# Kernel tuning notes

Measured on AMD Instinct MI355X. Metric: run time of the kernel, lower is better.

## Reference

```python
import jax, jax.numpy as jnp
import numpy as np

EPS = 1e-5
B, C_IN, T_IN = 512, 12, 5000
NF, HID, LAT = 32, 64, 32


def setup_inputs() -> dict:
    key = jax.random.key(0)
    ks = jax.random.split(key, 12)
    inp = {
        "x": jax.random.normal(ks[0], (B, C_IN, T_IN), dtype=jnp.float32),
        # conv stack
        "conv1_w": jax.random.normal(ks[1], (32, C_IN, 50), dtype=jnp.float32) * 0.05,
        "conv1_b": jnp.zeros((32,), dtype=jnp.float32),
        "bn1_g": jnp.ones((32,), dtype=jnp.float32),
        "bn1_b": jnp.zeros((32,), dtype=jnp.float32),
        "conv2_w": jax.random.normal(ks[2], (NF, 32, 25), dtype=jnp.float32) * 0.05,
        "conv2_b": jnp.zeros((NF,), dtype=jnp.float32),
        "bn2_g": jnp.ones((NF,), dtype=jnp.float32),
        "bn2_b": jnp.zeros((NF,), dtype=jnp.float32),
        # input projection + layernorm
        "proj_w": jax.random.normal(ks[3], (LAT, NF), dtype=jnp.float32) * 0.1,
        "proj_b": jnp.zeros((LAT,), dtype=jnp.float32),
        "ln_g": jnp.ones((LAT,), dtype=jnp.float32),
        "ln_b": jnp.zeros((LAT,), dtype=jnp.float32),
        # PLRNN recurrence params
        "A": jnp.eye(LAT, dtype=jnp.float32) * 0.9,
        "W": jax.random.normal(ks[4], (LAT, HID), dtype=jnp.float32) * 0.1,
        "h_bias": jnp.zeros((HID,), dtype=jnp.float32),
        # output projection
        "out_w": jax.random.normal(ks[5], (LAT, LAT), dtype=jnp.float32) * 0.1,
        "out_b": jnp.zeros((LAT,), dtype=jnp.float32),
    }
    return inp


def _conv1d(x, w, b, stride):
    # x: [B, C, T], w: [O, I, K]
    y = jax.lax.conv_general_dilated(
        x, w, window_strides=(stride,), padding="VALID",
        dimension_numbers=("NCH", "OIH", "NCH"))
    return y + b[None, :, None]


def _batchnorm_train(x, g, b):
    # training-mode BN over (batch, time) per channel; x: [B, C, T]
    mean = jnp.mean(x, axis=(0, 2), keepdims=True)
    var = jnp.mean((x - mean) ** 2, axis=(0, 2), keepdims=True)
    return (x - mean) * jax.lax.rsqrt(var + EPS) * g[None, :, None] + b[None, :, None]


def _layernorm(x, g, b):
    mean = jnp.mean(x, axis=-1, keepdims=True)
    var = jnp.mean((x - mean) ** 2, axis=-1, keepdims=True)
    return (x - mean) * jax.lax.rsqrt(var + EPS) * g + b


def reference(x, conv1_w, conv1_b, bn1_g, bn1_b, conv2_w, conv2_b, bn2_g, bn2_b,
              proj_w, proj_b, ln_g, ln_b, A, W, h_bias, out_w, out_b):
    # conv front-end
    y = jax.nn.relu(_batchnorm_train(_conv1d(x, conv1_w, conv1_b, 10), bn1_g, bn1_b))
    y = jax.nn.relu(_batchnorm_train(_conv1d(y, conv2_w, conv2_b, 5), bn2_g, bn2_b))
    y = jnp.transpose(y, (0, 2, 1))  # [B, T, NF], T = 95

    # input projection + LN, vectorized over all timesteps
    xt = _layernorm(jnp.einsum("btf,lf->btl", y, proj_w) + proj_b, ln_g, ln_b)  # [B, T, L]
    xs = jnp.transpose(xt, (1, 0, 2))  # [T, B, L] for scan

    def step(h, x_t):
        # h: [B, L]
        linear = h @ A.T
        nonlinear = jax.nn.relu(h @ W + h_bias) @ W.T
        h_new = linear + nonlinear + x_t
        return h_new, h_new

    h0 = jnp.zeros((x.shape[0], A.shape[0]), dtype=x.dtype)
    _, outputs = jax.lax.scan(step, h0, xs)  # [T, B, L]

    pooled = jnp.mean(outputs, axis=0)  # [B, L]
    return pooled @ out_w.T + out_b
```

## Files before the change

kernel.cpp:

```cpp
#include <hip/hip_runtime.h>

#define NB    512
#define CIN   12
#define TIN   5000
#define C1    32
#define T1    496
#define T2    95
#define LATD  32
#define HIDD  64

#define OFS_STATS 0
#define OFS_W1P   256
#define OFS_W2P   19456
#define OFS_Y1    45056
#define OFS_Y2    8171520
#define OFS_XS    OFS_Y1

__global__ void prep_kernel(const float* __restrict__ w1, const float* __restrict__ w2,
                            float* __restrict__ ws) {
    int idx = blockIdx.x * 256 + threadIdx.x;
    if (idx < 256) ws[idx] = 0.f;
    int j = idx - 256;
    if (j >= 0 && j < 19200) {
        int ic = j / 1600, r = j % 1600;
        int p = r / 160, rr = r % 160, jj = rr / 32, oc = rr % 32;
        ws[OFS_W1P + j] = w1[oc * 600 + ic * 50 + 10 * jj + p];
    }
    int j2 = idx - 19456;
    if (j2 >= 0 && j2 < 25600) {
        int ic = j2 / 800, r = j2 % 800;
        int p = r / 160, rr = r % 160, jj = rr / 32, oc = rr % 32;
        ws[OFS_W2P + j2] = w2[oc * 800 + ic * 25 + 5 * jj + p];
    }
}

__global__ __launch_bounds__(256, 4) void conv1_kernel(const float* __restrict__ x,
                                                       const float* __restrict__ b1,
                                                       float* __restrict__ ws) {
    const float* w1p = ws + OFS_W1P;
    float* y1 = ws + OFS_Y1;
    float* stats = ws + OFS_STATS;
    int b  = blockIdx.x >> 1;
    int t0 = (blockIdx.x & 1) * 256;
    int tid = threadIdx.x;
    int ocg = tid & 7, tg = tid >> 3;
    int oc0 = ocg * 4, lt0 = tg * 8;

    __shared__ __align__(16) float xs_s[2][2680];
    __shared__ __align__(16) float ws_s[2][1600];
    __shared__ float sred[256];

    float acc[4][8];
#pragma unroll
    for (int a = 0; a < 4; ++a)
#pragma unroll
        for (int c = 0; c < 8; ++c) acc[a][c] = 0.f;

    const float* xb = x + (size_t)b * (CIN * TIN) + t0 * 10;
    int nvalid = TIN - t0 * 10;

    float4 px[3];
    float4 pw[2];

    auto fetch = [&](int ic) {
#pragma unroll
        for (int j = 0; j < 3; ++j) {
            int i = tid + j * 256;
            if (i < 650) {
                int src = 4 * i;
                const float* gp = xb + ic * TIN + src;
                float4 v;
                if (src + 4 <= nvalid) {
                    v = *(const float4*)gp;
                } else {
                    v.x = (src + 0 < nvalid) ? gp[0] : 0.f;
                    v.y = (src + 1 < nvalid) ? gp[1] : 0.f;
                    v.z = (src + 2 < nvalid) ? gp[2] : 0.f;
                    v.w = (src + 3 < nvalid) ? gp[3] : 0.f;
                }
                px[j] = v;
            }
        }
#pragma unroll
        for (int j = 0; j < 2; ++j) {
            int i = tid + j * 256;
            if (i < 400) pw[j] = *(const float4*)(w1p + ic * 1600 + 4 * i);
        }
    };

    fetch(0);
    for (int ic = 0; ic < CIN; ++ic) {
        int cur = ic & 1;
        __syncthreads();
#pragma unroll
        for (int j = 0; j < 3; ++j) {
            int i = tid + j * 256;
            if (i < 650) {
                int g = 4 * i;
                int col = g / 10, p = g - 10 * col;
                float vals[4] = {px[j].x, px[j].y, px[j].z, px[j].w};
#pragma unroll
                for (int m = 0; m < 4; ++m) {
                    int pm = p + m;
                    int rr = (pm >= 10) ? pm - 10 : pm;
                    int cc = col + ((pm >= 10) ? 1 : 0);
                    xs_s[cur][rr * 268 + cc] = vals[m];
                }
            }
        }
#pragma unroll
        for (int j = 0; j < 2; ++j) {
            int i = tid + j * 256;
            if (i < 400) *(float4*)&ws_s[cur][4 * i] = pw[j];
        }
        if (ic + 1 < CIN) fetch(ic + 1);
        __syncthreads();

#pragma unroll 2
        for (int p = 0; p < 10; ++p) {
            const float* xr = &xs_s[cur][p * 268 + 8 * tg];
            float4 xa = *(const float4*)(xr);
            float4 xbv = *(const float4*)(xr + 4);
            float4 xc = *(const float4*)(xr + 8);
            float xv[12] = {xa.x, xa.y, xa.z, xa.w,
                            xbv.x, xbv.y, xbv.z, xbv.w,
                            xc.x, xc.y, xc.z, xc.w};
            const float* wr = &ws_s[cur][p * 160 + oc0];
            float4 w0 = *(const float4*)(wr);
            float4 w1v = *(const float4*)(wr + 32);
            float4 w2v = *(const float4*)(wr + 64);
            float4 w3v = *(const float4*)(wr + 96);
            float4 w4v = *(const float4*)(wr + 128);
            float wj[5][4] = {{w0.x, w0.y, w0.z, w0.w},
                              {w1v.x, w1v.y, w1v.z, w1v.w},
                              {w2v.x, w2v.y, w2v.z, w2v.w},
                              {w3v.x, w3v.y, w3v.z, w3v.w},
                              {w4v.x, w4v.y, w4v.z, w4v.w}};
#pragma unroll
            for (int j = 0; j < 5; ++j)
#pragma unroll
                for (int jt = 0; jt < 8; ++jt) {
                    float xx = xv[jt + j];
#pragma unroll
                    for (int jo = 0; jo < 4; ++jo)
                        acc[jo][jt] = fmaf(wj[j][jo], xx, acc[jo][jt]);
                }
        }
    }

    float bias[4];
#pragma unroll
    for (int jo = 0; jo < 4; ++jo) bias[jo] = b1[oc0 + jo];

    bool tvalid = (t0 + lt0) <= (T1 - 8);
    float psum[4], psq[4];
#pragma unroll
    for (int jo = 0; jo < 4; ++jo) {
        float s = 0.f, q = 0.f;
        if (tvalid) {
            float tmp[8];
#pragma unroll
            for (int jt = 0; jt < 8; ++jt) {
                float v = acc[jo][jt] + bias[jo];
                tmp[jt] = v; s += v; q = fmaf(v, v, q);
            }
            float* yrow = y1 + (size_t)(b * 32 + oc0 + jo) * T1 + t0 + lt0;
            float4 o0; o0.x = tmp[0]; o0.y = tmp[1]; o0.z = tmp[2]; o0.w = tmp[3];
            float4 o1; o1.x = tmp[4]; o1.y = tmp[5]; o1.z = tmp[6]; o1.w = tmp[7];
            *(float4*)yrow       = o0;
            *(float4*)(yrow + 4) = o1;
        }
        psum[jo] = s; psq[jo] = q;
    }
#pragma unroll
    for (int off = 32; off >= 8; off >>= 1) {
#pragma unroll
        for (int jo = 0; jo < 4; ++jo) {
            psum[jo] += __shfl_down(psum[jo], off, 64);
            psq[jo]  += __shfl_down(psq[jo],  off, 64);
        }
    }
    int lane = tid & 63, wvi = tid >> 6;
    if (lane < 8) {
#pragma unroll
        for (int jo = 0; jo < 4; ++jo) {
            sred[((wvi * 8 + lane) * 4 + jo) * 2 + 0] = psum[jo];
            sred[((wvi * 8 + lane) * 4 + jo) * 2 + 1] = psq[jo];
        }
    }
    __syncthreads();
    if (tid < 64) {
        int oc = tid >> 1, which = tid & 1;
        int og = oc >> 2, jo = oc & 3;
        float v = 0.f;
#pragma unroll
        for (int w = 0; w < 4; ++w)
            v += sred[((w * 8 + og) * 4 + jo) * 2 + which];
        atomicAdd(&stats[which * 32 + oc], v);
    }
}

__global__ __launch_bounds__(192, 2) void conv2_kernel(const float* __restrict__ b2,
                                                       const float* __restrict__ g1,
                                                       const float* __restrict__ be1,
                                                       float* __restrict__ ws) {
    const float* w2p = ws + OFS_W2P;
    const float* y1 = ws + OFS_Y1;
    float* y2 = ws + OFS_Y2;
    float* stats = ws + OFS_STATS;
    int b = blockIdx.x;
    int tid = threadIdx.x;
    int ocg = tid & 7, tg = tid >> 3;
    int oc0 = ocg * 4, lt0 = tg * 4;

    __shared__ __align__(16) float a1s[2][500];
    __shared__ __align__(16) float w2s[2][800];
    __shared__ float sred[192];
    __shared__ float bns[64];

    if (tid < 32) {
        float mean = stats[tid] * (1.f / 253952.f);
        float var  = stats[32 + tid] * (1.f / 253952.f) - mean * mean;
        float s = g1[tid] * rsqrtf(var + 1e-5f);
        bns[tid]      = s;
        bns[32 + tid] = be1[tid] - mean * s;
    }

    float acc[4][4];
#pragma unroll
    for (int a = 0; a < 4; ++a)
#pragma unroll
        for (int c = 0; c < 4; ++c) acc[a][c] = 0.f;

    float4 py, pw0, pw1;
    auto fetch = [&](int ic) {
        const float* yrow = y1 + (size_t)(b * 32 + ic) * T1;
        if (tid < 124) py = *(const float4*)(yrow + 4 * tid);
        pw0 = *(const float4*)(w2p + ic * 800 + 4 * tid);
        if (tid < 8) pw1 = *(const float4*)(w2p + ic * 800 + 4 * (tid + 192));
    };

    fetch(0);
    for (int ic = 0; ic < 32; ++ic) {
        int cur = ic & 1;
        __syncthreads();
        if (tid < 124) {
            float s1 = bns[ic], sh1 = bns[32 + ic];
            float4 v = py;
            float vals[4];
            vals[0] = fmaxf(fmaf(v.x, s1, sh1), 0.f);
            vals[1] = fmaxf(fmaf(v.y, s1, sh1), 0.f);
            vals[2] = fmaxf(fmaf(v.z, s1, sh1), 0.f);
            vals[3] = fmaxf(fmaf(v.w, s1, sh1), 0.f);
            int g = 4 * tid;
            int col = g / 5, p = g - 5 * col;
#pragma unroll
            for (int m = 0; m < 4; ++m) {
                int pm = p + m;
                int rr = (pm >= 5) ? pm - 5 : pm;
                int cc = col + ((pm >= 5) ? 1 : 0);
                a1s[cur][rr * 100 + cc] = vals[m];
            }
        }
        *(float4*)&w2s[cur][4 * tid] = pw0;
        if (tid < 8) *(float4*)&w2s[cur][4 * (tid + 192)] = pw1;
        if (ic + 1 < 32) fetch(ic + 1);
        __syncthreads();

#pragma unroll 2
        for (int p = 0; p < 5; ++p) {
            const float* xr = &a1s[cur][p * 100 + 4 * tg];
            float4 xa = *(const float4*)(xr);
            float4 xbv = *(const float4*)(xr + 4);
            float xv[8] = {xa.x, xa.y, xa.z, xa.w, xbv.x, xbv.y, xbv.z, xbv.w};
            const float* wr = &w2s[cur][p * 160 + oc0];
            float4 w0 = *(const float4*)(wr);
            float4 w1v = *(const float4*)(wr + 32);
            float4 w2v = *(const float4*)(wr + 64);
            float4 w3v = *(const float4*)(wr + 96);
            float4 w4v = *(const float4*)(wr + 128);
            float wj[5][4] = {{w0.x, w0.y, w0.z, w0.w},
                              {w1v.x, w1v.y, w1v.z, w1v.w},
                              {w2v.x, w2v.y, w2v.z, w2v.w},
                              {w3v.x, w3v.y, w3v.z, w3v.w},
                              {w4v.x, w4v.y, w4v.z, w4v.w}};
#pragma unroll
            for (int j = 0; j < 5; ++j)
#pragma unroll
                for (int jt = 0; jt < 4; ++jt) {
                    float xx = xv[jt + j];
#pragma unroll
                    for (int jo = 0; jo < 4; ++jo)
                        acc[jo][jt] = fmaf(wj[j][jo], xx, acc[jo][jt]);
                }
        }
    }

    float bias[4];
#pragma unroll
    for (int jo = 0; jo < 4; ++jo) bias[jo] = b2[oc0 + jo];

    float psum[4], psq[4];
#pragma unroll
    for (int jo = 0; jo < 4; ++jo) {
        float s = 0.f, q = 0.f;
#pragma unroll
        for (int jt = 0; jt < 4; ++jt) {
            int t2 = lt0 + jt;
            if (t2 < T2) {
                float v = acc[jo][jt] + bias[jo];
                y2[(size_t)(b * 32 + oc0 + jo) * T2 + t2] = v;
                s += v; q = fmaf(v, v, q);
            }
        }
        psum[jo] = s; psq[jo] = q;
    }
#pragma unroll
    for (int off = 32; off >= 8; off >>= 1) {
#pragma unroll
        for (int jo = 0; jo < 4; ++jo) {
            psum[jo] += __shfl_down(psum[jo], off, 64);
            psq[jo]  += __shfl_down(psq[jo],  off, 64);
        }
    }
    int lane = tid & 63, wvi = tid >> 6;
    if (lane < 8) {
#pragma unroll
        for (int jo = 0; jo < 4; ++jo) {
            sred[((wvi * 8 + lane) * 4 + jo) * 2 + 0] = psum[jo];
            sred[((wvi * 8 + lane) * 4 + jo) * 2 + 1] = psq[jo];
        }
    }
    __syncthreads();
    if (tid < 64) {
        int oc = tid >> 1, which = tid & 1;
        int og = oc >> 2, jo = oc & 3;
        float v = 0.f;
#pragma unroll
        for (int w = 0; w < 3; ++w)
            v += sred[((w * 8 + og) * 4 + jo) * 2 + which];
        atomicAdd(&stats[64 + which * 32 + oc], v);
    }
}

__global__ __launch_bounds__(256, 2) void proj_kernel(const float* __restrict__ g2,
                                                      const float* __restrict__ be2,
                                                      const float* __restrict__ pw,
                                                      const float* __restrict__ pb,
                                                      const float* __restrict__ lng,
                                                      const float* __restrict__ lnb,
                                                      float* __restrict__ ws) {
    int b = blockIdx.x;
    int tid = threadIdx.x;
    __shared__ float a2s[3040];
    __shared__ float pws[1056];
    __shared__ float bns2[64];
    const float* stats = ws + OFS_STATS;
    const float* y2 = ws + OFS_Y2 + (size_t)b * (32 * T2);
    float* xsg = ws + OFS_XS;

    if (tid < 32) {
        float mean = stats[64 + tid] * (1.f / 48640.f);
        float var  = stats[96 + tid] * (1.f / 48640.f) - mean * mean;
        float s = g2[tid] * rsqrtf(var + 1e-5f);
        bns2[tid]      = s;
        bns2[32 + tid] = be2[tid] - mean * s;
    }
    __syncthreads();

    for (int f = 0; f < 32; ++f) {
        float s2  = bns2[f];
        float sh2 = bns2[32 + f];
        if (tid < T2)
            a2s[f * T2 + tid] = fmaxf(fmaf(y2[f * T2 + tid], s2, sh2), 0.f);
    }
    for (int i = tid; i < 1024; i += 256)
        pws[(i >> 5) * 33 + (i & 31)] = pw[i];

    int l = tid & 31, ts = tid >> 5;
    float pbv = pb[l], lg = lng[l], lb = lnb[l];
    __syncthreads();

    for (int it = 0; it < 12; ++it) {
        int t = ts + 8 * it;
        if (t < T2) {
            float v = pbv;
#pragma unroll
            for (int f = 0; f < 32; ++f)
                v = fmaf(a2s[f * T2 + t], pws[l * 33 + f], v);
            float sum = v;
#pragma unroll
            for (int off = 16; off >= 1; off >>= 1) sum += __shfl_xor(sum, off, 64);
            float mean = sum * (1.f / 32.f);
            float d = v - mean;
            float q = d * d;
#pragma unroll
            for (int off = 16; off >= 1; off >>= 1) q += __shfl_xor(q, off, 64);
            float o = d * rsqrtf(q * (1.f / 32.f) + 1e-5f) * lg + lb;
            xsg[(size_t)t * (NB * 32) + b * 32 + l] = o;
        }
    }
}

__global__ __launch_bounds__(64)
__attribute__((amdgpu_waves_per_eu(1, 1)))
void scan_kernel(const float* __restrict__ Am,
                 const float* __restrict__ Wm,
                 const float* __restrict__ hbp,
                 const float* __restrict__ ow,
                 const float* __restrict__ ob,
                 const float* __restrict__ ws,
                 float* __restrict__ out) {
    int b = blockIdx.x;
    int lane = threadIdx.x;
    int l = lane & 31, half = lane >> 5;
    __shared__ __align__(16) float hs[32];
    __shared__ __align__(16) float hds[64];
    __shared__ float ows[1056];

    float Wc[32], WT[32], Ah[16];
#pragma unroll
    for (int j = 0; j < 32; ++j) Wc[j] = Wm[j * HIDD + lane];
#pragma unroll
    for (int m = 0; m < 32; ++m) WT[m] = Wm[l * HIDD + half * 32 + m];
#pragma unroll
    for (int j = 0; j < 16; ++j) Ah[j] = Am[l * 32 + half * 16 + j];
    float hbv = hbp[lane];
    for (int i = lane; i < 1024; i += 64)
        ows[(i >> 5) * 33 + (i & 31)] = ow[i];

    const float* xsg = ws + OFS_XS + b * 32;
    if (lane < 32) hs[l] = 0.f;
    float xv = xsg[l];
    float pool = 0.f;
    __syncthreads();

    for (int t = 0; t < T2; ++t) {
        __syncthreads();
        float4 hv[8];
#pragma unroll
        for (int q = 0; q < 8; ++q) hv[q] = *(const float4*)&hs[4 * q];
        float a0 = hbv, a1 = 0.f, a2 = 0.f, a3 = 0.f;
#pragma unroll
        for (int q = 0; q < 8; ++q) {
            a0 = fmaf(Wc[4 * q + 0], hv[q].x, a0);
            a1 = fmaf(Wc[4 * q + 1], hv[q].y, a1);
            a2 = fmaf(Wc[4 * q + 2], hv[q].z, a2);
            a3 = fmaf(Wc[4 * q + 3], hv[q].w, a3);
        }
        float hid = fmaxf((a0 + a1) + (a2 + a3), 0.f);
        float4 hl[4];
#pragma unroll
        for (int q = 0; q < 4; ++q) hl[q] = *(const float4*)&hs[half * 16 + 4 * q];
        float l0 = 0.f, l1 = 0.f;
#pragma unroll
        for (int q = 0; q < 4; ++q) {
            l0 = fmaf(Ah[4 * q + 0], hl[q].x, l0);
            l1 = fmaf(Ah[4 * q + 1], hl[q].y, l1);
            l0 = fmaf(Ah[4 * q + 2], hl[q].z, l0);
            l1 = fmaf(Ah[4 * q + 3], hl[q].w, l1);
        }
        float lin = l0 + l1;
        hds[lane] = hid;
        __syncthreads();
        float n0 = 0.f, n1 = 0.f, n2 = 0.f, n3 = 0.f;
#pragma unroll
        for (int q = 0; q < 8; ++q) {
            float4 d4 = *(const float4*)&hds[half * 32 + 4 * q];
            n0 = fmaf(WT[4 * q + 0], d4.x, n0);
            n1 = fmaf(WT[4 * q + 1], d4.y, n1);
            n2 = fmaf(WT[4 * q + 2], d4.z, n2);
            n3 = fmaf(WT[4 * q + 3], d4.w, n3);
        }
        float part = (n0 + n1) + (n2 + n3) + lin;
        part += __shfl_xor(part, 32, 64);
        float hnew = part + xv;
        pool += hnew;
        if (t + 1 < T2) xv = xsg[(size_t)(t + 1) * (NB * 32) + l];
        if (lane < 32) hs[l] = hnew;
    }

    __syncthreads();
    if (lane < 32) hs[l] = pool * (1.f / 95.f);
    __syncthreads();
    if (lane < 32) {
        float4 p0 = *(const float4*)&hs[0];
        float4 p1 = *(const float4*)&hs[4];
        float4 p2 = *(const float4*)&hs[8];
        float4 p3 = *(const float4*)&hs[12];
        float4 p4 = *(const float4*)&hs[16];
        float4 p5 = *(const float4*)&hs[20];
        float4 p6 = *(const float4*)&hs[24];
        float4 p7 = *(const float4*)&hs[28];
        float o = ob[l];
        const float* owr = &ows[l * 33];
        o = fmaf(owr[0],  p0.x, o); o = fmaf(owr[1],  p0.y, o);
        o = fmaf(owr[2],  p0.z, o); o = fmaf(owr[3],  p0.w, o);
        o = fmaf(owr[4],  p1.x, o); o = fmaf(owr[5],  p1.y, o);
        o = fmaf(owr[6],  p1.z, o); o = fmaf(owr[7],  p1.w, o);
        o = fmaf(owr[8],  p2.x, o); o = fmaf(owr[9],  p2.y, o);
        o = fmaf(owr[10], p2.z, o); o = fmaf(owr[11], p2.w, o);
        o = fmaf(owr[12], p3.x, o); o = fmaf(owr[13], p3.y, o);
        o = fmaf(owr[14], p3.z, o); o = fmaf(owr[15], p3.w, o);
        o = fmaf(owr[16], p4.x, o); o = fmaf(owr[17], p4.y, o);
        o = fmaf(owr[18], p4.z, o); o = fmaf(owr[19], p4.w, o);
        o = fmaf(owr[20], p5.x, o); o = fmaf(owr[21], p5.y, o);
        o = fmaf(owr[22], p5.z, o); o = fmaf(owr[23], p5.w, o);
        o = fmaf(owr[24], p6.x, o); o = fmaf(owr[25], p6.y, o);
        o = fmaf(owr[26], p6.z, o); o = fmaf(owr[27], p6.w, o);
        o = fmaf(owr[28], p7.x, o); o = fmaf(owr[29], p7.y, o);
        o = fmaf(owr[30], p7.z, o); o = fmaf(owr[31], p7.w, o);
        out[b * 32 + l] = o;
    }
}

extern "C" void kernel_launch(void* const* d_in, const int* in_sizes, int n_in,
                              void* d_out, int out_size, void* d_ws, size_t ws_size,
                              hipStream_t stream) {
    (void)in_sizes; (void)n_in; (void)out_size; (void)ws_size;
    const float* x   = (const float*)d_in[0];
    const float* w1  = (const float*)d_in[1];
    const float* b1  = (const float*)d_in[2];
    const float* g1  = (const float*)d_in[3];
    const float* be1 = (const float*)d_in[4];
    const float* w2  = (const float*)d_in[5];
    const float* b2  = (const float*)d_in[6];
    const float* g2  = (const float*)d_in[7];
    const float* be2 = (const float*)d_in[8];
    const float* pw  = (const float*)d_in[9];
    const float* pb  = (const float*)d_in[10];
    const float* lng = (const float*)d_in[11];
    const float* lnb = (const float*)d_in[12];
    const float* Am  = (const float*)d_in[13];
    const float* Wm  = (const float*)d_in[14];
    const float* hb  = (const float*)d_in[15];
    const float* ow  = (const float*)d_in[16];
    const float* ob  = (const float*)d_in[17];
    float* ws  = (float*)d_ws;
    float* out = (float*)d_out;

    prep_kernel<<<176, 256, 0, stream>>>(w1, w2, ws);
    conv1_kernel<<<1024, 256, 0, stream>>>(x, b1, ws);
    conv2_kernel<<<512, 192, 0, stream>>>(b2, g1, be1, ws);
    proj_kernel<<<512, 256, 0, stream>>>(g2, be2, pw, pb, lng, lnb, ws);
    scan_kernel<<<512, 64, 0, stream>>>(Am, Wm, hb, ow, ob, ws, out);
}
```

Baseline: 418.7 us.

## Restructure conv loops to one barrier per channel and split conv2 over time

Both conv kernels now stage the next input channel into the alternate shared buffer before computing the current one. That leaves a single barrier per channel iteration instead of two. conv2 is also split into two time-halves per batch (1024 blocks), each thread computing 2 outputs instead of 4, with launch bounds raised to 3 blocks per CU. The goal is less barrier stall and more parallelism/occupancy for conv2, at the cost of halo reloads of weights per block and fewer FMAs per loaded value.

```diff
diff --git a/kernel.cpp b/kernel.cpp
--- a/kernel.cpp
+++ b/kernel.cpp
@@ -88,10 +88,7 @@
         }
     };
 
-    fetch(0);
-    for (int ic = 0; ic < CIN; ++ic) {
-        int cur = ic & 1;
-        __syncthreads();
+    auto stage = [&](int cur) {
 #pragma unroll
         for (int j = 0; j < 3; ++j) {
             int i = tid + j * 256;
@@ -113,8 +110,17 @@
             int i = tid + j * 256;
             if (i < 400) *(float4*)&ws_s[cur][4 * i] = pw[j];
         }
-        if (ic + 1 < CIN) fetch(ic + 1);
-        __syncthreads();
+    };
+
+    fetch(0);
+    stage(0);
+    fetch(1);
+    __syncthreads();
+
+    for (int ic = 0; ic < CIN; ++ic) {
+        int cur = ic & 1;
+        if (ic + 1 < CIN) stage(cur ^ 1);
+        if (ic + 2 < CIN) fetch(ic + 2);
 
 #pragma unroll 2
         for (int p = 0; p < 10; ++p) {
@@ -146,6 +152,7 @@
                         acc[jo][jt] = fmaf(wj[j][jo], xx, acc[jo][jt]);
                 }
         }
+        __syncthreads();
     }
 
     float bias[4];
@@ -200,7 +207,7 @@
     }
 }
 
-__global__ __launch_bounds__(192, 2) void conv2_kernel(const float* __restrict__ b2,
+__global__ __launch_bounds__(192, 3) void conv2_kernel(const float* __restrict__ b2,
                                                        const float* __restrict__ g1,
                                                        const float* __restrict__ be1,
                                                        float* __restrict__ ws) {
@@ -208,12 +215,15 @@
     const float* y1 = ws + OFS_Y1;
     float* y2 = ws + OFS_Y2;
     float* stats = ws + OFS_STATS;
-    int b = blockIdx.x;
+    int b  = blockIdx.x >> 1;
+    int th = blockIdx.x & 1;
+    int t0 = th * 48;
+    int base = 5 * t0;
     int tid = threadIdx.x;
     int ocg = tid & 7, tg = tid >> 3;
-    int oc0 = ocg * 4, lt0 = tg * 4;
-
-    __shared__ __align__(16) float a1s[2][500];
+    int oc0 = ocg * 4, lt0 = tg * 2;
+
+    __shared__ __align__(16) float a1s[2][280];
     __shared__ __align__(16) float w2s[2][800];
     __shared__ float sred[192];
     __shared__ float bns[64];
@@ -226,32 +236,40 @@
         bns[32 + tid] = be1[tid] - mean * s;
     }
 
-    float acc[4][4];
+    float acc[4][2];
 #pragma unroll
     for (int a = 0; a < 4; ++a)
 #pragma unroll
-        for (int c = 0; c < 4; ++c) acc[a][c] = 0.f;
+        for (int c = 0; c < 2; ++c) acc[a][c] = 0.f;
 
     float4 py, pw0, pw1;
     auto fetch = [&](int ic) {
-        const float* yrow = y1 + (size_t)(b * 32 + ic) * T1;
-        if (tid < 124) py = *(const float4*)(yrow + 4 * tid);
+        const float* yrow = y1 + (size_t)(b * 32 + ic) * T1 + base;
+        if (tid < 65) {
+            int src = 4 * tid;
+            float4 v;
+            if (base + src + 4 <= T1) {
+                v = *(const float4*)(yrow + src);
+            } else {
+                v.x = (base + src + 0 < T1) ? yrow[src + 0] : 0.f;
+                v.y = (base + src + 1 < T1) ? yrow[src + 1] : 0.f;
+                v.z = (base + src + 2 < T1) ? yrow[src + 2] : 0.f;
+                v.w = (base + src + 3 < T1) ? yrow[src + 3] : 0.f;
+            }
+            py = v;
+        }
         pw0 = *(const float4*)(w2p + ic * 800 + 4 * tid);
         if (tid < 8) pw1 = *(const float4*)(w2p + ic * 800 + 4 * (tid + 192));
     };
 
-    fetch(0);
-    for (int ic = 0; ic < 32; ++ic) {
-        int cur = ic & 1;
-        __syncthreads();
-        if (tid < 124) {
+    auto stage = [&](int ic, int cur) {
+        if (tid < 65) {
             float s1 = bns[ic], sh1 = bns[32 + ic];
-            float4 v = py;
             float vals[4];
-            vals[0] = fmaxf(fmaf(v.x, s1, sh1), 0.f);
-            vals[1] = fmaxf(fmaf(v.y, s1, sh1), 0.f);
-            vals[2] = fmaxf(fmaf(v.z, s1, sh1), 0.f);
-            vals[3] = fmaxf(fmaf(v.w, s1, sh1), 0.f);
+            vals[0] = fmaxf(fmaf(py.x, s1, sh1), 0.f);
+            vals[1] = fmaxf(fmaf(py.y, s1, sh1), 0.f);
+            vals[2] = fmaxf(fmaf(py.z, s1, sh1), 0.f);
+            vals[3] = fmaxf(fmaf(py.w, s1, sh1), 0.f);
             int g = 4 * tid;
             int col = g / 5, p = g - 5 * col;
 #pragma unroll
@@ -259,20 +277,31 @@
                 int pm = p + m;
                 int rr = (pm >= 5) ? pm - 5 : pm;
                 int cc = col + ((pm >= 5) ? 1 : 0);
-                a1s[cur][rr * 100 + cc] = vals[m];
+                a1s[cur][rr * 56 + cc] = vals[m];
             }
         }
         *(float4*)&w2s[cur][4 * tid] = pw0;
         if (tid < 8) *(float4*)&w2s[cur][4 * (tid + 192)] = pw1;
-        if (ic + 1 < 32) fetch(ic + 1);
-        __syncthreads();
+    };
+
+    fetch(0);
+    __syncthreads();
+    stage(0, 0);
+    fetch(1);
+    __syncthreads();
+
+    for (int ic = 0; ic < 32; ++ic) {
+        int cur = ic & 1;
+        if (ic + 1 < 32) stage(ic + 1, cur ^ 1);
+        if (ic + 2 < 32) fetch(ic + 2);
 
 #pragma unroll 2
         for (int p = 0; p < 5; ++p) {
-            const float* xr = &a1s[cur][p * 100 + 4 * tg];
-            float4 xa = *(const float4*)(xr);
-            float4 xbv = *(const float4*)(xr + 4);
-            float xv[8] = {xa.x, xa.y, xa.z, xa.w, xbv.x, xbv.y, xbv.z, xbv.w};
+            const float* xr = &a1s[cur][p * 56 + 2 * tg];
+            float2 x01 = *(const float2*)(xr);
+            float2 x23 = *(const float2*)(xr + 2);
+            float2 x45 = *(const float2*)(xr + 4);
+            float xv[6] = {x01.x, x01.y, x23.x, x23.y, x45.x, x45.y};
             const float* wr = &w2s[cur][p * 160 + oc0];
             float4 w0 = *(const float4*)(wr);
             float4 w1v = *(const float4*)(wr + 32);
@@ -287,13 +316,14 @@
 #pragma unroll
             for (int j = 0; j < 5; ++j)
 #pragma unroll
-                for (int jt = 0; jt < 4; ++jt) {
+                for (int jt = 0; jt < 2; ++jt) {
                     float xx = xv[jt + j];
 #pragma unroll
                     for (int jo = 0; jo < 4; ++jo)
                         acc[jo][jt] = fmaf(wj[j][jo], xx, acc[jo][jt]);
                 }
         }
+        __syncthreads();
     }
 
     float bias[4];
@@ -305,8 +335,8 @@
     for (int jo = 0; jo < 4; ++jo) {
         float s = 0.f, q = 0.f;
 #pragma unroll
-        for (int jt = 0; jt < 4; ++jt) {
-            int t2 = lt0 + jt;
+        for (int jt = 0; jt < 2; ++jt) {
+            int t2 = t0 + lt0 + jt;
             if (t2 < T2) {
                 float v = acc[jo][jt] + bias[jo];
                 y2[(size_t)(b * 32 + oc0 + jo) * T2 + t2] = v;
@@ -541,7 +571,7 @@
 
     prep_kernel<<<176, 256, 0, stream>>>(w1, w2, ws);
     conv1_kernel<<<1024, 256, 0, stream>>>(x, b1, ws);
-    conv2_kernel<<<512, 192, 0, stream>>>(b2, g1, be1, ws);
+    conv2_kernel<<<1024, 192, 0, stream>>>(b2, g1, be1, ws);
     proj_kernel<<<512, 256, 0, stream>>>(g2, be2, pw, pb, lng, lnb, ws);
     scan_kernel<<<512, 64, 0, stream>>>(Am, Wm, hb, ow, ob, ws, out);
 }
```

Result: slower. 431.7 us (+3.1%).

## Fuse projection+layernorm into scan kernel and software-pipeline conv1 staging

Applied to the files above, without the earlier changes.

Removes the separate proj_kernel and computes BN2+ReLU, input projection and layernorm inside each scan block, keeping the per-timestep inputs in shared memory. This drops one launch plus the global write and strided reread of the [T,B,L] intermediate. Separately, conv1's channel loop is restructured so the next channel is staged into shared memory before the current channel's compute, with one barrier per iteration instead of two. The cost is that the projection now runs on only 64 threads per block, and the scan kernel uses more shared memory and registers.

```diff
diff --git a/kernel.cpp b/kernel.cpp
--- a/kernel.cpp
+++ b/kernel.cpp
@@ -14,7 +14,6 @@
 #define OFS_W2P   19456
 #define OFS_Y1    45056
 #define OFS_Y2    8171520
-#define OFS_XS    OFS_Y1
 
 __global__ void prep_kernel(const float* __restrict__ w1, const float* __restrict__ w2,
                             float* __restrict__ ws) {
@@ -88,10 +87,7 @@
         }
     };
 
-    fetch(0);
-    for (int ic = 0; ic < CIN; ++ic) {
-        int cur = ic & 1;
-        __syncthreads();
+    auto stage = [&](int cur) {
 #pragma unroll
         for (int j = 0; j < 3; ++j) {
             int i = tid + j * 256;
@@ -113,8 +109,17 @@
             int i = tid + j * 256;
             if (i < 400) *(float4*)&ws_s[cur][4 * i] = pw[j];
         }
-        if (ic + 1 < CIN) fetch(ic + 1);
-        __syncthreads();
+    };
+
+    fetch(0);
+    stage(0);
+    fetch(1);
+    __syncthreads();
+
+    for (int ic = 0; ic < CIN; ++ic) {
+        int cur = ic & 1;
+        if (ic + 1 < CIN) stage(cur ^ 1);
+        if (ic + 2 < CIN) fetch(ic + 2);
 
 #pragma unroll 2
         for (int p = 0; p < 10; ++p) {
@@ -146,6 +151,7 @@
                         acc[jo][jt] = fmaf(wj[j][jo], xx, acc[jo][jt]);
                 }
         }
+        __syncthreads();
     }
 
     float bias[4];
@@ -343,68 +349,15 @@
     }
 }
 
-__global__ __launch_bounds__(256, 2) void proj_kernel(const float* __restrict__ g2,
-                                                      const float* __restrict__ be2,
-                                                      const float* __restrict__ pw,
-                                                      const float* __restrict__ pb,
-                                                      const float* __restrict__ lng,
-                                                      const float* __restrict__ lnb,
-                                                      float* __restrict__ ws) {
-    int b = blockIdx.x;
-    int tid = threadIdx.x;
-    __shared__ float a2s[3040];
-    __shared__ float pws[1056];
-    __shared__ float bns2[64];
-    const float* stats = ws + OFS_STATS;
-    const float* y2 = ws + OFS_Y2 + (size_t)b * (32 * T2);
-    float* xsg = ws + OFS_XS;
-
-    if (tid < 32) {
-        float mean = stats[64 + tid] * (1.f / 48640.f);
-        float var  = stats[96 + tid] * (1.f / 48640.f) - mean * mean;
-        float s = g2[tid] * rsqrtf(var + 1e-5f);
-        bns2[tid]      = s;
-        bns2[32 + tid] = be2[tid] - mean * s;
-    }
-    __syncthreads();
-
-    for (int f = 0; f < 32; ++f) {
-        float s2  = bns2[f];
-        float sh2 = bns2[32 + f];
-        if (tid < T2)
-            a2s[f * T2 + tid] = fmaxf(fmaf(y2[f * T2 + tid], s2, sh2), 0.f);
-    }
-    for (int i = tid; i < 1024; i += 256)
-        pws[(i >> 5) * 33 + (i & 31)] = pw[i];
-
-    int l = tid & 31, ts = tid >> 5;
-    float pbv = pb[l], lg = lng[l], lb = lnb[l];
-    __syncthreads();
-
-    for (int it = 0; it < 12; ++it) {
-        int t = ts + 8 * it;
-        if (t < T2) {
-            float v = pbv;
-#pragma unroll
-            for (int f = 0; f < 32; ++f)
-                v = fmaf(a2s[f * T2 + t], pws[l * 33 + f], v);
-            float sum = v;
-#pragma unroll
-            for (int off = 16; off >= 1; off >>= 1) sum += __shfl_xor(sum, off, 64);
-            float mean = sum * (1.f / 32.f);
-            float d = v - mean;
-            float q = d * d;
-#pragma unroll
-            for (int off = 16; off >= 1; off >>= 1) q += __shfl_xor(q, off, 64);
-            float o = d * rsqrtf(q * (1.f / 32.f) + 1e-5f) * lg + lb;
-            xsg[(size_t)t * (NB * 32) + b * 32 + l] = o;
-        }
-    }
-}
-
 __global__ __launch_bounds__(64)
 __attribute__((amdgpu_waves_per_eu(1, 1)))
-void scan_kernel(const float* __restrict__ Am,
+void scan_kernel(const float* __restrict__ g2,
+                 const float* __restrict__ be2,
+                 const float* __restrict__ pwm,
+                 const float* __restrict__ pb,
+                 const float* __restrict__ lng,
+                 const float* __restrict__ lnb,
+                 const float* __restrict__ Am,
                  const float* __restrict__ Wm,
                  const float* __restrict__ hbp,
                  const float* __restrict__ ow,
@@ -414,9 +367,74 @@
     int b = blockIdx.x;
     int lane = threadIdx.x;
     int l = lane & 31, half = lane >> 5;
+    __shared__ __align__(16) float y2a[95 * 36];
+    __shared__ __align__(16) float xsl[95 * 32];
     __shared__ __align__(16) float hs[32];
     __shared__ __align__(16) float hds[64];
     __shared__ float ows[1056];
+    __shared__ float bns2[64];
+
+    const float* stats = ws + OFS_STATS;
+    if (lane < 32) {
+        float mean = stats[64 + lane] * (1.f / 48640.f);
+        float var  = stats[96 + lane] * (1.f / 48640.f) - mean * mean;
+        float s = g2[lane] * rsqrtf(var + 1e-5f);
+        bns2[lane]      = s;
+        bns2[32 + lane] = be2[lane] - mean * s;
+    }
+    float pwreg[32];
+#pragma unroll
+    for (int k = 0; k < 8; ++k) {
+        float4 v = *(const float4*)(pwm + l * 32 + 4 * k);
+        pwreg[4 * k + 0] = v.x; pwreg[4 * k + 1] = v.y;
+        pwreg[4 * k + 2] = v.z; pwreg[4 * k + 3] = v.w;
+    }
+    float pbv = pb[l], lgv = lng[l], lbv = lnb[l];
+    for (int i = lane; i < 1024; i += 64)
+        ows[(i >> 5) * 33 + (i & 31)] = ow[i];
+    __syncthreads();
+
+    const float* y2 = ws + OFS_Y2 + (size_t)b * (32 * T2);
+#pragma unroll
+    for (int it = 0; it < 12; ++it) {
+        int i4 = lane + it * 64;
+        if (i4 < 760) {
+            float4 v = *(const float4*)(y2 + 4 * i4);
+            float vals[4] = {v.x, v.y, v.z, v.w};
+#pragma unroll
+            for (int m = 0; m < 4; ++m) {
+                int e = 4 * i4 + m;
+                int f = e / 95, t = e - 95 * f;
+                y2a[t * 36 + f] = fmaxf(fmaf(vals[m], bns2[f], bns2[32 + f]), 0.f);
+            }
+        }
+    }
+    __syncthreads();
+
+    for (int it = 0; it < 48; ++it) {
+        int t = 2 * it + half;
+        if (t < T2) {
+            const float* yr = &y2a[t * 36];
+            float v = pbv;
+#pragma unroll
+            for (int k = 0; k < 8; ++k) {
+                float4 ya = *(const float4*)(yr + 4 * k);
+                v = fmaf(ya.x, pwreg[4 * k + 0], v);
+                v = fmaf(ya.y, pwreg[4 * k + 1], v);
+                v = fmaf(ya.z, pwreg[4 * k + 2], v);
+                v = fmaf(ya.w, pwreg[4 * k + 3], v);
+            }
+            float sum = v;
+#pragma unroll
+            for (int off = 16; off >= 1; off >>= 1) sum += __shfl_xor(sum, off, 64);
+            float mean = sum * (1.f / 32.f);
+            float d = v - mean;
+            float q = d * d;
+#pragma unroll
+            for (int off = 16; off >= 1; off >>= 1) q += __shfl_xor(q, off, 64);
+            xsl[t * 32 + l] = d * rsqrtf(q * (1.f / 32.f) + 1e-5f) * lgv + lbv;
+        }
+    }
 
     float Wc[32], WT[32], Ah[16];
 #pragma unroll
@@ -426,14 +444,11 @@
 #pragma unroll
     for (int j = 0; j < 16; ++j) Ah[j] = Am[l * 32 + half * 16 + j];
     float hbv = hbp[lane];
-    for (int i = lane; i < 1024; i += 64)
-        ows[(i >> 5) * 33 + (i & 31)] = ow[i];
-
-    const float* xsg = ws + OFS_XS + b * 32;
+
     if (lane < 32) hs[l] = 0.f;
-    float xv = xsg[l];
     float pool = 0.f;
     __syncthreads();
+    float xv = xsl[l];
 
     for (int t = 0; t < T2; ++t) {
         __syncthreads();
@@ -476,7 +491,7 @@
         part += __shfl_xor(part, 32, 64);
         float hnew = part + xv;
         pool += hnew;
-        if (t + 1 < T2) xv = xsg[(size_t)(t + 1) * (NB * 32) + l];
+        if (t + 1 < T2) xv = xsl[(t + 1) * 32 + l];
         if (lane < 32) hs[l] = hnew;
     }
 
@@ -542,6 +557,6 @@
     prep_kernel<<<176, 256, 0, stream>>>(w1, w2, ws);
     conv1_kernel<<<1024, 256, 0, stream>>>(x, b1, ws);
     conv2_kernel<<<512, 192, 0, stream>>>(b2, g1, be1, ws);
-    proj_kernel<<<512, 256, 0, stream>>>(g2, be2, pw, pb, lng, lnb, ws);
-    scan_kernel<<<512, 64, 0, stream>>>(Am, Wm, hb, ow, ob, ws, out);
+    scan_kernel<<<512, 64, 0, stream>>>(g2, be2, pw, pb, lng, lnb,
+                                        Am, Wm, hb, ow, ob, ws, out);
 }
```

Result: slower. 436.8 us (+4.3%).
